# Kernel tuning notes

Hardware: AMD Instinct MI355X
Metric: run time of the kernel (lower is better)

The kernel has to match this reference:

```python
import jax, jax.numpy as jnp
import numpy as np

DIM = 512
HEADS = 8        # MultiHeadAttention default heads=8 (init 'heads' arg actually sets dim_head)
DIM_HEAD = 64    # from AttentionLayers heads=64 passed positionally as dim_head
HIDDEN = HEADS * DIM_HEAD  # 512
EPS = 1e-5


def setup_inputs() -> dict:
    key = jax.random.key(0)
    ks = jax.random.split(key, 8)
    s = 1.0 / np.sqrt(DIM)
    return {
        "x": jax.random.normal(ks[0], (4, 2048, DIM), dtype=jnp.float32),
        "ln_g": jnp.ones((DIM,), dtype=jnp.float32),
        "ln_b": jnp.zeros((DIM,), dtype=jnp.float32),
        "Wq": jax.random.normal(ks[1], (DIM, HIDDEN), dtype=jnp.float32) * s,
        "Wk": jax.random.normal(ks[2], (DIM, HIDDEN), dtype=jnp.float32) * s,
        "Wv": jax.random.normal(ks[3], (DIM, HIDDEN), dtype=jnp.float32) * s,
        "Wo": jax.random.normal(ks[4], (HIDDEN, DIM), dtype=jnp.float32) * s,
        "bo": jnp.zeros((DIM,), dtype=jnp.float32),
    }


def reference(x, ln_g, ln_b, Wq, Wk, Wv, Wo, bo):
    b, n, d = x.shape
    residual = x
    # pre-norm LayerNorm
    mu = jnp.mean(x, axis=-1, keepdims=True)
    var = jnp.mean((x - mu) ** 2, axis=-1, keepdims=True)
    xn = (x - mu) * jax.lax.rsqrt(var + EPS) * ln_g + ln_b
    # QKV projections (no bias), split into heads: [b, s, h, dh]
    q = (xn @ Wq).reshape(b, n, HEADS, DIM_HEAD)
    k = (xn @ Wk).reshape(b, n, HEADS, DIM_HEAD)
    v = (xn @ Wv).reshape(b, n, HEADS, DIM_HEAD)
    scale = HIDDEN ** (-0.5)  # note: scales by hidden_dim, not dim_head (faithful)
    scores = jnp.einsum('bihd,bjhd->bhij', q, k) * scale  # [b,h,i,j] full matrix
    attn = jax.nn.softmax(scores, axis=-1)
    out = jnp.einsum('bhij,bjhd->bihd', attn, v).reshape(b, n, HIDDEN)
    out = out @ Wo + bo
    # residual; the subsequent FFN layer's output is discarded in the source
    return out + residual
```

## Files before the change

kernel.cpp:

```cpp
#include <hip/hip_runtime.h>
#include <hip/hip_bf16.h>

#define DIM 512
#define SEQ 2048
#define BATCH 4
#define NHEADS 8
#define DH 64
#define NROWS (BATCH * SEQ)
#define LN_EPS 1e-5f

typedef __hip_bfloat16 bf16;
typedef __attribute__((ext_vector_type(8))) short short8;
typedef __attribute__((ext_vector_type(4))) float f32x4;

#define MFMA16(a, b, c) __builtin_amdgcn_mfma_f32_16x16x32_bf16((a), (b), (c), 0, 0, 0)

#if __has_builtin(__builtin_amdgcn_exp2f)
#define EXP2(x) __builtin_amdgcn_exp2f(x)
#else
#define EXP2(x) exp2f(x)
#endif

#if defined(__has_builtin)
#if __has_builtin(__builtin_amdgcn_global_load_lds)
#define HAS_GLDS 1
#endif
#endif

__device__ __forceinline__ void glds16(const bf16* g, bf16* l) {
#ifdef HAS_GLDS
  __builtin_amdgcn_global_load_lds((const __attribute__((address_space(1))) void*)g,
                                   (__attribute__((address_space(3))) void*)l, 16, 0, 0);
#else
  *reinterpret_cast<uint4*>(l) = *reinterpret_cast<const uint4*>(g);
#endif
}

__device__ __forceinline__ void store_bf16x4(bf16* p, float a, float b, float c, float d) {
  bf16 tmp[4] = {__float2bfloat16(a), __float2bfloat16(b), __float2bfloat16(c),
                 __float2bfloat16(d)};
  *reinterpret_cast<ushort4*>(p) = *reinterpret_cast<const ushort4*>(tmp);
}

#define B2F(us) __uint_as_float(((unsigned)(us)) << 16)

#define Q_SCALE_LOG2E 0.06375872f

__global__ void setup_kernel(const float* __restrict__ x, const float* __restrict__ gamma,
                             const float* __restrict__ beta, bf16* __restrict__ xn,
                             const float* __restrict__ Wq, const float* __restrict__ Wk,
                             const float* __restrict__ Wv, const float* __restrict__ Wo,
                             bf16* __restrict__ Wt) {
  const int t = threadIdx.x;
  if (blockIdx.x < NROWS / 4) {
    const int row = blockIdx.x * 4 + (t >> 6);
    const int l = t & 63;
    const float4* xr = reinterpret_cast<const float4*>(x + (size_t)row * DIM);
    const float4 v0 = xr[l * 2];
    const float4 v1 = xr[l * 2 + 1];
    float s = (v0.x + v0.y + v0.z + v0.w) + (v1.x + v1.y + v1.z + v1.w);
    float ss = v0.x * v0.x + v0.y * v0.y + v0.z * v0.z + v0.w * v0.w + v1.x * v1.x +
               v1.y * v1.y + v1.z * v1.z + v1.w * v1.w;
#pragma unroll
    for (int off = 1; off < 64; off <<= 1) {
      s += __shfl_xor(s, off);
      ss += __shfl_xor(ss, off);
    }
    const float mu = s * (1.0f / DIM);
    const float rs = rsqrtf(ss * (1.0f / DIM) - mu * mu + LN_EPS);
    const float4 g0 = reinterpret_cast<const float4*>(gamma)[l * 2];
    const float4 g1 = reinterpret_cast<const float4*>(gamma)[l * 2 + 1];
    const float4 b0 = reinterpret_cast<const float4*>(beta)[l * 2];
    const float4 b1 = reinterpret_cast<const float4*>(beta)[l * 2 + 1];
    bf16* o = xn + (size_t)row * DIM + l * 8;
    store_bf16x4(o, (v0.x - mu) * rs * g0.x + b0.x, (v0.y - mu) * rs * g0.y + b0.y,
                 (v0.z - mu) * rs * g0.z + b0.z, (v0.w - mu) * rs * g0.w + b0.w);
    store_bf16x4(o + 4, (v1.x - mu) * rs * g1.x + b1.x, (v1.y - mu) * rs * g1.y + b1.y,
                 (v1.z - mu) * rs * g1.z + b1.z, (v1.w - mu) * rs * g1.w + b1.w);
  } else {
    __shared__ float tile[32][33];
    const int idx = blockIdx.x - NROWS / 4;
    const int bx = idx & 15, by = (idx >> 4) & 15, z = idx >> 8;
    const float* __restrict__ W = (z == 0) ? Wq : (z == 1) ? Wk : (z == 2) ? Wv : Wo;
    const float scale = (z == 0) ? Q_SCALE_LOG2E : 1.0f;
    bf16* __restrict__ dst = Wt + (size_t)z * DIM * DIM;
    const int tx = t & 31, ty = t >> 5;
#pragma unroll
    for (int i = 0; i < 32; i += 8)
      tile[ty + i][tx] = W[(size_t)(by * 32 + ty + i) * DIM + bx * 32 + tx];
    __syncthreads();
#pragma unroll
    for (int i = 0; i < 32; i += 8)
      dst[(size_t)(bx * 32 + ty + i) * DIM + by * 32 + tx] =
          __float2bfloat16(tile[tx][ty + i] * scale);
  }
}

__launch_bounds__(256, 3)
__global__ void gemm_qkv_kernel(const bf16* __restrict__ A, const bf16* __restrict__ Bt,
                                bf16* __restrict__ qo, bf16* __restrict__ ko,
                                bf16* __restrict__ vto) {
  const int m0 = blockIdx.x * 128, n0g = blockIdx.y * 128;
  __shared__ __align__(16) char smem[128 * 136 * 2];
  bf16* const sA = (bf16*)smem;
  bf16* const sB = (bf16*)(smem + 16384);
  bf16* const sT = (bf16*)smem;
  const int t = threadIdx.x, w = t >> 6, l = t & 63;
  const int r = l & 15, g = l >> 4;
  const int wm = w >> 1, wn = w & 1;
  const int crow = w * 32 + (l >> 2);
  const int ccol = (l & 3) * 8;
  const bf16* gA = A + (size_t)(m0 + crow) * DIM + ccol;
  const bf16* gB = Bt + (size_t)(n0g + crow) * DIM + ccol;
  const int loff = w * 1024 + l * 8;
  f32x4 acc[4][4] = {};
  glds16(gA, sA + loff);
  glds16(gA + 16 * DIM, sA + loff + 512);
  glds16(gB, sB + loff);
  glds16(gB + 16 * DIM, sB + loff + 512);
  const int NK = DIM / 32;
  for (int ks = 0; ks < NK; ks++) {
    const int cur = ks & 1;
    __syncthreads();
    if (ks + 1 < NK) {
      const int k0n = (ks + 1) * 32;
      glds16(gA + k0n, sA + (1 - cur) * 4096 + loff);
      glds16(gA + 16 * DIM + k0n, sA + (1 - cur) * 4096 + loff + 512);
      glds16(gB + k0n, sB + (1 - cur) * 4096 + loff);
      glds16(gB + 16 * DIM + k0n, sB + (1 - cur) * 4096 + loff + 512);
    }
    short8 af[4], bfv[4];
#pragma unroll
    for (int i = 0; i < 4; i++)
      af[i] = *reinterpret_cast<const short8*>(
          &sA[cur * 4096 + (wm * 64 + i * 16 + r) * 32 + g * 8]);
#pragma unroll
    for (int j = 0; j < 4; j++)
      bfv[j] = *reinterpret_cast<const short8*>(
          &sB[cur * 4096 + (wn * 64 + j * 16 + r) * 32 + g * 8]);
#pragma unroll
    for (int i = 0; i < 4; i++)
#pragma unroll
      for (int j = 0; j < 4; j++) acc[i][j] = MFMA16(af[i], bfv[j], acc[i][j]);
  }
  const int z = n0g >> 9;
  const int b = m0 / SEQ;
  if (z != 2) {
    bf16* __restrict__ outp = (z == 0) ? qo : ko;
    const int nc0 = (n0g & 511) + wn * 64;
#pragma unroll
    for (int i = 0; i < 4; i++)
#pragma unroll
      for (int j = 0; j < 4; j++)
#pragma unroll
        for (int reg = 0; reg < 4; reg++) {
          const int m = m0 + wm * 64 + i * 16 + g * 4 + reg;
          const int col = nc0 + j * 16 + r;
          outp[(size_t)m * DIM + col] = __float2bfloat16(acc[i][j][reg]);
        }
  } else {
    __syncthreads();
#pragma unroll
    for (int i = 0; i < 4; i++)
#pragma unroll
      for (int j = 0; j < 4; j++)
        store_bf16x4(&sT[(wn * 64 + j * 16 + r) * 136 + wm * 64 + i * 16 + g * 4],
                     acc[i][j][0], acc[i][j][1], acc[i][j][2], acc[i][j][3]);
    __syncthreads();
    const int dr = t >> 1;
    const int mc = (t & 1) * 64;
    const int dcol = (n0g & 511) + dr;
    bf16* dst = vto + ((size_t)b * DIM + dcol) * SEQ + (m0 - b * SEQ) + mc;
#pragma unroll
    for (int uu = 0; uu < 8; uu++)
      *reinterpret_cast<uint4*>(dst + uu * 8) =
          *reinterpret_cast<const uint4*>(&sT[dr * 136 + mc + uu * 8]);
  }
}

template <bool SPLIT>
__launch_bounds__(256, 4)
__global__ void attn_kernel(const bf16* __restrict__ q, const bf16* __restrict__ k,
                            const bf16* __restrict__ vt, bf16* __restrict__ opart,
                            float* __restrict__ lpart) {
  const int bh = blockIdx.x, jh = blockIdx.y, it = blockIdx.z;
  const int b = bh >> 3, h = bh & 7;
  const int t = threadIdx.x, wv = t >> 6, l = t & 63;
  const int r = l & 15, g = l >> 4;
  __shared__ __align__(16) bf16 sK[64 * 64];
  __shared__ __align__(16) bf16 sV[64 * 64];
  __shared__ __align__(16) bf16 sPt[4][2][16][72];
  const int i0 = it * 128 + wv * 32;
  const bf16* qp = q + ((size_t)(b * SEQ) + i0 + r) * DIM + h * DH;
  short8 qf[2][2];
#pragma unroll
  for (int s = 0; s < 2; s++)
#pragma unroll
    for (int kc = 0; kc < 2; kc++)
      qf[s][kc] = *reinterpret_cast<const short8*>(qp + s * 16 * DIM + kc * 32 + g * 8);
  f32x4 oacc[2][4] = {};
  float lsum[2] = {0.f, 0.f};
  const int jbase = SPLIT ? jh * (SEQ / 2) : 0;
  const int srow8 = l >> 3;
  const int u = ((l & 7) - srow8) & 7;
  const bf16* kg = k + ((size_t)(b * SEQ) + jbase + wv * 16 + srow8) * DIM + h * DH + u * 8;
  const bf16* vg = vt + ((size_t)(b * DIM) + h * DH + wv * 16 + srow8) * SEQ + jbase + u * 8;
  const int loff = wv * 1024 + l * 8;
  const int e0 = 64 * r + 8 * ((g + r) & 7);
  const int e1 = 64 * r + 8 * ((4 + g + r) & 7);
  const int NJ = SPLIT ? (SEQ / 2) / 64 : SEQ / 64;
  for (int jt = 0; jt < NJ; jt++) {
    const int j0 = jt * 64;
#pragma unroll
    for (int cc = 0; cc < 2; cc++) {
      glds16(kg + (size_t)(j0 + cc * 8) * DIM, sK + loff + cc * 512);
      glds16(vg + (size_t)(cc * 8) * SEQ + j0, sV + loff + cc * 512);
    }
    __syncthreads();
    f32x4 st[2][4];
#pragma unroll
    for (int c = 0; c < 4; c++) {
      const short8 kf0 = *reinterpret_cast<const short8*>(sK + 1024 * c + e0);
      const short8 kf1 = *reinterpret_cast<const short8*>(sK + 1024 * c + e1);
#pragma unroll
      for (int s = 0; s < 2; s++) {
        f32x4 a = {0.f, 0.f, 0.f, 0.f};
        a = MFMA16(kf0, qf[s][0], a);
        a = MFMA16(kf1, qf[s][1], a);
        st[s][c] = a;
      }
    }
#pragma unroll
    for (int s = 0; s < 2; s++)
#pragma unroll
      for (int c = 0; c < 4; c++) {
        const float p0 = EXP2(st[s][c][0]);
        const float p1 = EXP2(st[s][c][1]);
        const float p2 = EXP2(st[s][c][2]);
        const float p3 = EXP2(st[s][c][3]);
        lsum[s] += (p0 + p1) + (p2 + p3);
        store_bf16x4(&sPt[wv][s][r][c * 16 + g * 4], p0, p1, p2, p3);
      }
#pragma unroll
    for (int kc2 = 0; kc2 < 2; kc2++) {
      short8 pf[2];
#pragma unroll
      for (int s = 0; s < 2; s++)
        pf[s] = *reinterpret_cast<const short8*>(&sPt[wv][s][r][kc2 * 32 + g * 8]);
      const int ev = (kc2 == 0) ? e0 : e1;
#pragma unroll
      for (int dt = 0; dt < 4; dt++) {
        const short8 vf = *reinterpret_cast<const short8*>(sV + 1024 * dt + ev);
#pragma unroll
        for (int s = 0; s < 2; s++) oacc[s][dt] = MFMA16(vf, pf[s], oacc[s][dt]);
      }
    }
    __syncthreads();
  }
#pragma unroll
  for (int s = 0; s < 2; s++) {
    lsum[s] += __shfl_xor(lsum[s], 16);
    lsum[s] += __shfl_xor(lsum[s], 32);
  }
  const size_t obase = ((size_t)(SPLIT ? jh * 32 : 0) + bh) * SEQ;
#pragma unroll
  for (int s = 0; s < 2; s++) {
    const int i = i0 + s * 16 + r;
    if (l < 16) lpart[obase + i] = lsum[s];
#pragma unroll
    for (int dt = 0; dt < 4; dt++)
      store_bf16x4(opart + (obase + i) * 64 + dt * 16 + g * 4, oacc[s][dt][0], oacc[s][dt][1],
                   oacc[s][dt][2], oacc[s][dt][3]);
  }
  if (!SPLIT) {
    const size_t obase1 = ((size_t)32 + bh) * SEQ;
#pragma unroll
    for (int s = 0; s < 2; s++) {
      const int i = i0 + s * 16 + r;
      if (l < 16) lpart[obase1 + i] = 0.f;
#pragma unroll
      for (int dt = 0; dt < 4; dt++)
        store_bf16x4(opart + (obase1 + i) * 64 + dt * 16 + g * 4, 0.f, 0.f, 0.f, 0.f);
    }
  }
}

__launch_bounds__(256, 2)
__global__ void gemm_proj_kernel(const bf16* __restrict__ opart, const float* __restrict__ lpart,
                                 const bf16* __restrict__ Bt, const float* __restrict__ bo,
                                 const float* __restrict__ x, float* __restrict__ out) {
  const int m0 = blockIdx.x * 128, n0 = blockIdx.y * 64;
  __shared__ __align__(16) bf16 sA[128 * 32];
  __shared__ __align__(16) bf16 sB[64 * 32];
  const int t = threadIdx.x, w = t >> 6, l = t & 63;
  const int r = l & 15, g = l >> 4;
  const int wm = w >> 1, wn = w & 1;
  const int arow = t >> 2;
  const int acol = (t & 3) * 8;
  const bf16* gB = Bt + (size_t)(n0 + arow) * DIM + acol;
  f32x4 acc[4][2] = {};
  const int NK = DIM / 32;
  for (int ks = 0; ks < NK; ks++) {
    const int k0 = ks * 32;
    const int h = k0 >> 6;
    const int d0 = (k0 & 63) + acol;
    uint4 areg[2];
#pragma unroll
    for (int c = 0; c < 2; c++) {
      const int m = m0 + c * 64 + arow;
      const int bb = m >> 11, ii = m & 2047;
      const size_t row0 = ((size_t)(bb * 8 + h)) * SEQ + ii;
      const size_t row1 = row0 + (size_t)32 * SEQ;
      const uint4 A0 = *reinterpret_cast<const uint4*>(opart + row0 * 64 + d0);
      const uint4 A1 = *reinterpret_cast<const uint4*>(opart + row1 * 64 + d0);
      const float inv = 1.0f / (lpart[row0] + lpart[row1]);
      const ushort* a0 = (const ushort*)&A0;
      const ushort* a1 = (const ushort*)&A1;
      bf16 rr[8];
#pragma unroll
      for (int e = 0; e < 8; e++)
        rr[e] = __float2bfloat16((B2F(a0[e]) + B2F(a1[e])) * inv);
      areg[c] = *reinterpret_cast<const uint4*>(rr);
    }
    const uint4 breg = *reinterpret_cast<const uint4*>(gB + k0);
    __syncthreads();
    *reinterpret_cast<uint4*>(&sA[(0 * 64 + arow) * 32 + acol]) = areg[0];
    *reinterpret_cast<uint4*>(&sA[(1 * 64 + arow) * 32 + acol]) = areg[1];
    *reinterpret_cast<uint4*>(&sB[arow * 32 + acol]) = breg;
    __syncthreads();
    short8 af[4], bfv[2];
#pragma unroll
    for (int i = 0; i < 4; i++)
      af[i] = *reinterpret_cast<const short8*>(&sA[(wm * 64 + i * 16 + r) * 32 + g * 8]);
#pragma unroll
    for (int j = 0; j < 2; j++)
      bfv[j] = *reinterpret_cast<const short8*>(&sB[(wn * 32 + j * 16 + r) * 32 + g * 8]);
#pragma unroll
    for (int i = 0; i < 4; i++)
#pragma unroll
      for (int j = 0; j < 2; j++) acc[i][j] = MFMA16(af[i], bfv[j], acc[i][j]);
  }
#pragma unroll
  for (int i = 0; i < 4; i++)
#pragma unroll
    for (int j = 0; j < 2; j++)
#pragma unroll
      for (int reg = 0; reg < 4; reg++) {
        const int m = m0 + wm * 64 + i * 16 + g * 4 + reg;
        const int col = n0 + wn * 32 + j * 16 + r;
        out[(size_t)m * DIM + col] = acc[i][j][reg] + bo[col] + x[(size_t)m * DIM + col];
      }
}

extern "C" void kernel_launch(void* const* d_in, const int* in_sizes, int n_in,
                              void* d_out, int out_size, void* d_ws, size_t ws_size,
                              hipStream_t stream) {
  (void)in_sizes; (void)n_in; (void)out_size;
  const float* x    = (const float*)d_in[0];
  const float* ln_g = (const float*)d_in[1];
  const float* ln_b = (const float*)d_in[2];
  const float* Wq   = (const float*)d_in[3];
  const float* Wk   = (const float*)d_in[4];
  const float* Wv   = (const float*)d_in[5];
  const float* Wo   = (const float*)d_in[6];
  const float* bo   = (const float*)d_in[7];
  float* out = (float*)d_out;
  char* ws = (char*)d_ws;
  bf16* xn  = (bf16*)(ws);
  bf16* wt  = (bf16*)(ws + (8u << 20));
  bf16* qb  = (bf16*)(ws + (10u << 20));
  bf16* kb  = (bf16*)(ws + (18u << 20));
  bf16* vtb = (bf16*)(ws + (26u << 20));
  bf16* opart = (bf16*)(ws + (34u << 20));
  float* lpart = (float*)(ws + (50u << 20));
  const bool split = ws_size >= ((50u << 20) + (1u << 19));

  setup_kernel<<<NROWS / 4 + 1024, 256, 0, stream>>>(x, ln_g, ln_b, xn, Wq, Wk, Wv, Wo, wt);
  gemm_qkv_kernel<<<dim3(NROWS / 128, (3 * DIM) / 128), 256, 0, stream>>>(xn, wt, qb, kb, vtb);
  if (split) {
    attn_kernel<true><<<dim3(BATCH * NHEADS, 2, SEQ / 128), 256, 0, stream>>>(
        qb, kb, vtb, opart, lpart);
  } else {
    attn_kernel<false><<<dim3(BATCH * NHEADS, 1, SEQ / 128), 256, 0, stream>>>(
        qb, kb, vtb, opart, lpart);
  }
  gemm_proj_kernel<<<dim3(NROWS / 128, DIM / 64), 256, 0, stream>>>(
      opart, lpart, wt + 3 * DIM * DIM, bo, x, out);
}
```

Before: 167.3 us.

## Rewrite attention inner loop with 32x32 MFMA, register P, double-buffered K/V

The attention kernel switches from 16x16x32 to 32x32x16 bf16 MFMA, with each wave handling 64 query rows, so a block covers 256 rows and the grid's z dimension is halved. The probability tile is repacked in registers with cross-half shuffles instead of a round trip through shared memory. K/V tiles are double-buffered so the next tile's global-to-LDS load overlaps compute, using a single raw barrier per iteration. The aim is higher MFMA throughput and fewer LDS accesses and syncs, at the cost of more registers (launch bounds drop to 2 blocks per CU) and fewer blocks in the grid.

```diff
diff --git a/kernel.cpp b/kernel.cpp
--- a/kernel.cpp
+++ b/kernel.cpp
@@ -12,8 +12,10 @@
 typedef __hip_bfloat16 bf16;
 typedef __attribute__((ext_vector_type(8))) short short8;
 typedef __attribute__((ext_vector_type(4))) float f32x4;
+typedef __attribute__((ext_vector_type(16))) float f32x16;
 
 #define MFMA16(a, b, c) __builtin_amdgcn_mfma_f32_16x16x32_bf16((a), (b), (c), 0, 0, 0)
+#define MFMA32(a, b, c) __builtin_amdgcn_mfma_f32_32x32x16_bf16((a), (b), (c), 0, 0, 0)
 
 #if __has_builtin(__builtin_amdgcn_exp2f)
 #define EXP2(x) __builtin_amdgcn_exp2f(x)
@@ -42,7 +44,23 @@
   *reinterpret_cast<ushort4*>(p) = *reinterpret_cast<const ushort4*>(tmp);
 }
 
+__device__ __forceinline__ unsigned pk2(float a, float b) {
+  union { bf16 h[2]; unsigned u; } x;
+  x.h[0] = __float2bfloat16(a);
+  x.h[1] = __float2bfloat16(b);
+  return x.u;
+}
+
+__device__ __forceinline__ short8 mk8(unsigned a, unsigned b, unsigned c, unsigned d) {
+  union { unsigned u[4]; short8 s; } x;
+  x.u[0] = a; x.u[1] = b; x.u[2] = c; x.u[3] = d;
+  return x.s;
+}
+
 #define B2F(us) __uint_as_float(((unsigned)(us)) << 16)
+
+#define BARRIER() asm volatile("s_barrier" ::: "memory")
+#define WAITVM0() asm volatile("s_waitcnt vmcnt(0)" ::: "memory")
 
 #define Q_SCALE_LOG2E 0.06375872f
 
@@ -179,108 +197,141 @@
 }
 
 template <bool SPLIT>
-__launch_bounds__(256, 4)
+__launch_bounds__(256, 2)
 __global__ void attn_kernel(const bf16* __restrict__ q, const bf16* __restrict__ k,
                             const bf16* __restrict__ vt, bf16* __restrict__ opart,
                             float* __restrict__ lpart) {
   const int bh = blockIdx.x, jh = blockIdx.y, it = blockIdx.z;
   const int b = bh >> 3, h = bh & 7;
   const int t = threadIdx.x, wv = t >> 6, l = t & 63;
-  const int r = l & 15, g = l >> 4;
-  __shared__ __align__(16) bf16 sK[64 * 64];
-  __shared__ __align__(16) bf16 sV[64 * 64];
-  __shared__ __align__(16) bf16 sPt[4][2][16][72];
-  const int i0 = it * 128 + wv * 32;
-  const bf16* qp = q + ((size_t)(b * SEQ) + i0 + r) * DIM + h * DH;
-  short8 qf[2][2];
-#pragma unroll
-  for (int s = 0; s < 2; s++)
-#pragma unroll
-    for (int kc = 0; kc < 2; kc++)
-      qf[s][kc] = *reinterpret_cast<const short8*>(qp + s * 16 * DIM + kc * 32 + g * 8);
-  f32x4 oacc[2][4] = {};
-  float lsum[2] = {0.f, 0.f};
+  const int c2 = l & 31, h2 = l >> 5;
+  __shared__ __align__(16) bf16 sK[2][64 * 64];
+  __shared__ __align__(16) bf16 sV[2][64 * 64];
+  const int i0w = it * 256 + wv * 64;
   const int jbase = SPLIT ? jh * (SEQ / 2) : 0;
+
   const int srow8 = l >> 3;
   const int u = ((l & 7) - srow8) & 7;
   const bf16* kg = k + ((size_t)(b * SEQ) + jbase + wv * 16 + srow8) * DIM + h * DH + u * 8;
   const bf16* vg = vt + ((size_t)(b * DIM) + h * DH + wv * 16 + srow8) * SEQ + jbase + u * 8;
   const int loff = wv * 1024 + l * 8;
-  const int e0 = 64 * r + 8 * ((g + r) & 7);
-  const int e1 = 64 * r + 8 * ((4 + g + r) & 7);
+#pragma unroll
+  for (int cc = 0; cc < 2; cc++) {
+    glds16(kg + (size_t)(cc * 8) * DIM, &sK[0][loff + cc * 512]);
+    glds16(vg + (size_t)(cc * 8) * SEQ, &sV[0][loff + cc * 512]);
+  }
+
+  const bf16* qp = q + ((size_t)(b * SEQ) + i0w + c2) * DIM + h * DH + h2 * 8;
+  short8 qf[2][4];
+#pragma unroll
+  for (int x = 0; x < 2; x++)
+#pragma unroll
+    for (int kk = 0; kk < 4; kk++)
+      qf[x][kk] = *reinterpret_cast<const short8*>(qp + x * 32 * DIM + kk * 16);
+
+  int eo[4];
+#pragma unroll
+  for (int x = 0; x < 4; x++) eo[x] = c2 * 64 + 8 * ((2 * x + h2 + c2) & 7);
+
+  f32x16 oacc[2][2] = {};
+  float lsum[2] = {0.f, 0.f};
   const int NJ = SPLIT ? (SEQ / 2) / 64 : SEQ / 64;
+
   for (int jt = 0; jt < NJ; jt++) {
-    const int j0 = jt * 64;
-#pragma unroll
-    for (int cc = 0; cc < 2; cc++) {
-      glds16(kg + (size_t)(j0 + cc * 8) * DIM, sK + loff + cc * 512);
-      glds16(vg + (size_t)(cc * 8) * SEQ + j0, sV + loff + cc * 512);
-    }
-    __syncthreads();
-    f32x4 st[2][4];
-#pragma unroll
-    for (int c = 0; c < 4; c++) {
-      const short8 kf0 = *reinterpret_cast<const short8*>(sK + 1024 * c + e0);
-      const short8 kf1 = *reinterpret_cast<const short8*>(sK + 1024 * c + e1);
-#pragma unroll
-      for (int s = 0; s < 2; s++) {
-        f32x4 a = {0.f, 0.f, 0.f, 0.f};
-        a = MFMA16(kf0, qf[s][0], a);
-        a = MFMA16(kf1, qf[s][1], a);
-        st[s][c] = a;
+    WAITVM0();
+    BARRIER();
+    if (jt + 1 < NJ) {
+      const int j0n = (jt + 1) * 64;
+      const int bn = (jt + 1) & 1;
+#pragma unroll
+      for (int cc = 0; cc < 2; cc++) {
+        glds16(kg + (size_t)(j0n + cc * 8) * DIM, &sK[bn][loff + cc * 512]);
+        glds16(vg + (size_t)(cc * 8) * SEQ + j0n, &sV[bn][loff + cc * 512]);
       }
     }
-#pragma unroll
-    for (int s = 0; s < 2; s++)
-#pragma unroll
-      for (int c = 0; c < 4; c++) {
-        const float p0 = EXP2(st[s][c][0]);
-        const float p1 = EXP2(st[s][c][1]);
-        const float p2 = EXP2(st[s][c][2]);
-        const float p3 = EXP2(st[s][c][3]);
-        lsum[s] += (p0 + p1) + (p2 + p3);
-        store_bf16x4(&sPt[wv][s][r][c * 16 + g * 4], p0, p1, p2, p3);
+    const bf16* sKb = sK[jt & 1];
+    const bf16* sVb = sV[jt & 1];
+#pragma unroll
+    for (int jb = 0; jb < 2; jb++) {
+      short8 kf[4];
+#pragma unroll
+      for (int kk = 0; kk < 4; kk++)
+        kf[kk] = *reinterpret_cast<const short8*>(sKb + jb * 2048 + eo[kk]);
+      f32x16 st[2] = {};
+#pragma unroll
+      for (int kk = 0; kk < 4; kk++) {
+        st[0] = MFMA32(kf[kk], qf[0][kk], st[0]);
+        st[1] = MFMA32(kf[kk], qf[1][kk], st[1]);
       }
-#pragma unroll
-    for (int kc2 = 0; kc2 < 2; kc2++) {
-      short8 pf[2];
-#pragma unroll
-      for (int s = 0; s < 2; s++)
-        pf[s] = *reinterpret_cast<const short8*>(&sPt[wv][s][r][kc2 * 32 + g * 8]);
-      const int ev = (kc2 == 0) ? e0 : e1;
-#pragma unroll
-      for (int dt = 0; dt < 4; dt++) {
-        const short8 vf = *reinterpret_cast<const short8*>(sV + 1024 * dt + ev);
-#pragma unroll
-        for (int s = 0; s < 2; s++) oacc[s][dt] = MFMA16(vf, pf[s], oacc[s][dt]);
+      short8 pf[2][2];
+#pragma unroll
+      for (int x = 0; x < 2; x++) {
+        float p[16];
+#pragma unroll
+        for (int e = 0; e < 16; e++) p[e] = EXP2(st[x][e]);
+        lsum[x] += ((((p[0] + p[1]) + (p[2] + p[3])) + ((p[4] + p[5]) + (p[6] + p[7]))) +
+                    (((p[8] + p[9]) + (p[10] + p[11])) + ((p[12] + p[13]) + (p[14] + p[15]))));
+        unsigned W[4][2];
+#pragma unroll
+        for (int a = 0; a < 4; a++)
+#pragma unroll
+          for (int w = 0; w < 2; w++) W[a][w] = pk2(p[4 * a + 2 * w], p[4 * a + 2 * w + 1]);
+#pragma unroll
+        for (int k2 = 0; k2 < 2; k2++) {
+          unsigned F0, F1, F2, F3;
+          {
+            const unsigned We = W[2 * k2][0], Wo = W[2 * k2 + 1][0];
+            const unsigned te = __shfl_xor(We, 32), to = __shfl_xor(Wo, 32);
+            F0 = h2 ? to : We;
+            F2 = h2 ? Wo : te;
+          }
+          {
+            const unsigned We = W[2 * k2][1], Wo = W[2 * k2 + 1][1];
+            const unsigned te = __shfl_xor(We, 32), to = __shfl_xor(Wo, 32);
+            F1 = h2 ? to : We;
+            F3 = h2 ? Wo : te;
+          }
+          pf[x][k2] = mk8(F0, F1, F2, F3);
+        }
       }
-    }
-    __syncthreads();
-  }
-#pragma unroll
-  for (int s = 0; s < 2; s++) {
-    lsum[s] += __shfl_xor(lsum[s], 16);
-    lsum[s] += __shfl_xor(lsum[s], 32);
+#pragma unroll
+      for (int j2 = 0; j2 < 2; j2++) {
+#pragma unroll
+        for (int db = 0; db < 2; db++) {
+          const short8 vf =
+              *reinterpret_cast<const short8*>(sVb + db * 2048 + eo[2 * jb + j2]);
+          oacc[0][db] = MFMA32(vf, pf[0][j2], oacc[0][db]);
+          oacc[1][db] = MFMA32(vf, pf[1][j2], oacc[1][db]);
+        }
+      }
+    }
   }
   const size_t obase = ((size_t)(SPLIT ? jh * 32 : 0) + bh) * SEQ;
 #pragma unroll
-  for (int s = 0; s < 2; s++) {
-    const int i = i0 + s * 16 + r;
-    if (l < 16) lpart[obase + i] = lsum[s];
-#pragma unroll
-    for (int dt = 0; dt < 4; dt++)
-      store_bf16x4(opart + (obase + i) * 64 + dt * 16 + g * 4, oacc[s][dt][0], oacc[s][dt][1],
-                   oacc[s][dt][2], oacc[s][dt][3]);
+  for (int x = 0; x < 2; x++) {
+    lsum[x] += __shfl_xor(lsum[x], 32);
+    const int i = i0w + x * 32 + c2;
+    if (l < 32) lpart[obase + i] = lsum[x];
+#pragma unroll
+    for (int db = 0; db < 2; db++)
+#pragma unroll
+      for (int rr = 0; rr < 4; rr++)
+        store_bf16x4(opart + (obase + i) * 64 + db * 32 + rr * 8 + h2 * 4,
+                     oacc[x][db][4 * rr + 0], oacc[x][db][4 * rr + 1],
+                     oacc[x][db][4 * rr + 2], oacc[x][db][4 * rr + 3]);
   }
   if (!SPLIT) {
     const size_t obase1 = ((size_t)32 + bh) * SEQ;
 #pragma unroll
-    for (int s = 0; s < 2; s++) {
-      const int i = i0 + s * 16 + r;
-      if (l < 16) lpart[obase1 + i] = 0.f;
-#pragma unroll
-      for (int dt = 0; dt < 4; dt++)
-        store_bf16x4(opart + (obase1 + i) * 64 + dt * 16 + g * 4, 0.f, 0.f, 0.f, 0.f);
+    for (int x = 0; x < 2; x++) {
+      const int i = i0w + x * 32 + c2;
+      if (l < 32) lpart[obase1 + i] = 0.f;
+#pragma unroll
+      for (int db = 0; db < 2; db++)
+#pragma unroll
+        for (int rr = 0; rr < 4; rr++)
+          store_bf16x4(opart + (obase1 + i) * 64 + db * 32 + rr * 8 + h2 * 4, 0.f, 0.f, 0.f,
+                       0.f);
     }
   }
 }
@@ -378,10 +429,10 @@
   setup_kernel<<<NROWS / 4 + 1024, 256, 0, stream>>>(x, ln_g, ln_b, xn, Wq, Wk, Wv, Wo, wt);
   gemm_qkv_kernel<<<dim3(NROWS / 128, (3 * DIM) / 128), 256, 0, stream>>>(xn, wt, qb, kb, vtb);
   if (split) {
-    attn_kernel<true><<<dim3(BATCH * NHEADS, 2, SEQ / 128), 256, 0, stream>>>(
+    attn_kernel<true><<<dim3(BATCH * NHEADS, 2, SEQ / 256), 256, 0, stream>>>(
         qb, kb, vtb, opart, lpart);
   } else {
-    attn_kernel<false><<<dim3(BATCH * NHEADS, 1, SEQ / 128), 256, 0, stream>>>(
+    attn_kernel<false><<<dim3(BATCH * NHEADS, 1, SEQ / 256), 256, 0, stream>>>(
         qb, kb, vtb, opart, lpart);
   }
   gemm_proj_kernel<<<dim3(NROWS / 128, DIM / 64), 256, 0, stream>>>(
```

New measurement: 170.0 us. No clear change (+1.6%).

## Double-buffer K/V tiles in attention loop to overlap loads with MFMA

Applied to the files above, without the earlier changes.

Splits the K and V shared-memory tiles into two buffers and issues the global-to-LDS loads for the next tile right after the barrier, so they overlap with the current tile's score and PV computation. Raw s_waitcnt/s_barrier asm replaces __syncthreads, and launch bounds drop from 4 to 3 blocks per CU to cover the larger LDS footprint. The prologue is odd: it loads the first K chunk twice to the same slot and patches the second chunk inside the loop at jt==0. Fewer resident blocks and hand-written barriers could cut latency hiding or risk races.

```diff
diff --git a/kernel.cpp b/kernel.cpp
--- a/kernel.cpp
+++ b/kernel.cpp
@@ -43,6 +43,9 @@
 }
 
 #define B2F(us) __uint_as_float(((unsigned)(us)) << 16)
+
+#define BARRIER() asm volatile("s_barrier" ::: "memory")
+#define WAITVM0() asm volatile("s_waitcnt vmcnt(0)" ::: "memory")
 
 #define Q_SCALE_LOG2E 0.06375872f
 
@@ -179,7 +182,7 @@
 }
 
 template <bool SPLIT>
-__launch_bounds__(256, 4)
+__launch_bounds__(256, 3)
 __global__ void attn_kernel(const bf16* __restrict__ q, const bf16* __restrict__ k,
                             const bf16* __restrict__ vt, bf16* __restrict__ opart,
                             float* __restrict__ lpart) {
@@ -187,8 +190,8 @@
   const int b = bh >> 3, h = bh & 7;
   const int t = threadIdx.x, wv = t >> 6, l = t & 63;
   const int r = l & 15, g = l >> 4;
-  __shared__ __align__(16) bf16 sK[64 * 64];
-  __shared__ __align__(16) bf16 sV[64 * 64];
+  __shared__ __align__(16) bf16 sK[2][64 * 64];
+  __shared__ __align__(16) bf16 sV[2][64 * 64];
   __shared__ __align__(16) bf16 sPt[4][2][16][72];
   const int i0 = it * 128 + wv * 32;
   const bf16* qp = q + ((size_t)(b * SEQ) + i0 + r) * DIM + h * DH;
@@ -209,19 +212,33 @@
   const int e0 = 64 * r + 8 * ((g + r) & 7);
   const int e1 = 64 * r + 8 * ((4 + g + r) & 7);
   const int NJ = SPLIT ? (SEQ / 2) / 64 : SEQ / 64;
+#pragma unroll
+  for (int cc = 0; cc < 2; cc++) {
+    glds16(kg, &sK[0][loff + cc * 512]);
+    glds16(vg + (size_t)(cc * 8) * SEQ, &sV[0][loff + cc * 512]);
+  }
   for (int jt = 0; jt < NJ; jt++) {
-    const int j0 = jt * 64;
-#pragma unroll
-    for (int cc = 0; cc < 2; cc++) {
-      glds16(kg + (size_t)(j0 + cc * 8) * DIM, sK + loff + cc * 512);
-      glds16(vg + (size_t)(cc * 8) * SEQ + j0, sV + loff + cc * 512);
-    }
-    __syncthreads();
+    if (jt == 0) {
+      glds16(kg + (size_t)8 * DIM, &sK[0][loff + 512]);
+    }
+    WAITVM0();
+    BARRIER();
+    if (jt + 1 < NJ) {
+      const int j0n = (jt + 1) * 64;
+      const int bn = (jt + 1) & 1;
+#pragma unroll
+      for (int cc = 0; cc < 2; cc++) {
+        glds16(kg + (size_t)(j0n + cc * 8) * DIM, &sK[bn][loff + cc * 512]);
+        glds16(vg + (size_t)(cc * 8) * SEQ + j0n, &sV[bn][loff + cc * 512]);
+      }
+    }
+    const bf16* sKb = sK[jt & 1];
+    const bf16* sVb = sV[jt & 1];
     f32x4 st[2][4];
 #pragma unroll
     for (int c = 0; c < 4; c++) {
-      const short8 kf0 = *reinterpret_cast<const short8*>(sK + 1024 * c + e0);
-      const short8 kf1 = *reinterpret_cast<const short8*>(sK + 1024 * c + e1);
+      const short8 kf0 = *reinterpret_cast<const short8*>(sKb + 1024 * c + e0);
+      const short8 kf1 = *reinterpret_cast<const short8*>(sKb + 1024 * c + e1);
 #pragma unroll
       for (int s = 0; s < 2; s++) {
         f32x4 a = {0.f, 0.f, 0.f, 0.f};
@@ -250,12 +267,12 @@
       const int ev = (kc2 == 0) ? e0 : e1;
 #pragma unroll
       for (int dt = 0; dt < 4; dt++) {
-        const short8 vf = *reinterpret_cast<const short8*>(sV + 1024 * dt + ev);
+        const short8 vf = *reinterpret_cast<const short8*>(sVb + 1024 * dt + ev);
 #pragma unroll
         for (int s = 0; s < 2; s++) oacc[s][dt] = MFMA16(vf, pf[s], oacc[s][dt]);
       }
     }
-    __syncthreads();
+    BARRIER();
   }
 #pragma unroll
   for (int s = 0; s < 2; s++) {
```

Measured after the change: 174.4 us. 1.04x slower.

## Double-buffer K/V tiles in attention and retile output projection GEMM

Applied to the files above, without the earlier changes.

The attention loop now walks the keys in 32-wide tiles held in two LDS buffers. The next tile is prefetched with global_load_lds while the current one is computed, and a single raw s_barrier plus vmcnt wait per iteration replaces the two __syncthreads. The output projection GEMM changes from 128x64 to 64x128 tiles and loads B directly into LDS. Its launch bound rises to 4 blocks per CU. The raw barrier relies on each wave waiting for its own LDS writes, and with smaller tiles there are more loop iterations to pay overhead on.

```diff
diff --git a/kernel.cpp b/kernel.cpp
--- a/kernel.cpp
+++ b/kernel.cpp
@@ -43,6 +43,9 @@
 }
 
 #define B2F(us) __uint_as_float(((unsigned)(us)) << 16)
+
+#define BARRIER() asm volatile("s_barrier" ::: "memory")
+#define WAITVM0() asm volatile("s_waitcnt vmcnt(0)" ::: "memory")
 
 #define Q_SCALE_LOG2E 0.06375872f
 
@@ -187,8 +190,8 @@
   const int b = bh >> 3, h = bh & 7;
   const int t = threadIdx.x, wv = t >> 6, l = t & 63;
   const int r = l & 15, g = l >> 4;
-  __shared__ __align__(16) bf16 sK[64 * 64];
-  __shared__ __align__(16) bf16 sV[64 * 64];
+  __shared__ __align__(16) bf16 sK[2][32 * 64];
+  __shared__ __align__(16) bf16 sV[2][64 * 32];
   __shared__ __align__(16) bf16 sPt[4][2][16][72];
   const int i0 = it * 128 + wv * 32;
   const bf16* qp = q + ((size_t)(b * SEQ) + i0 + r) * DIM + h * DH;
@@ -201,27 +204,35 @@
   f32x4 oacc[2][4] = {};
   float lsum[2] = {0.f, 0.f};
   const int jbase = SPLIT ? jh * (SEQ / 2) : 0;
-  const int srow8 = l >> 3;
-  const int u = ((l & 7) - srow8) & 7;
-  const bf16* kg = k + ((size_t)(b * SEQ) + jbase + wv * 16 + srow8) * DIM + h * DH + u * 8;
-  const bf16* vg = vt + ((size_t)(b * DIM) + h * DH + wv * 16 + srow8) * SEQ + jbase + u * 8;
-  const int loff = wv * 1024 + l * 8;
-  const int e0 = 64 * r + 8 * ((g + r) & 7);
-  const int e1 = 64 * r + 8 * ((4 + g + r) & 7);
-  const int NJ = SPLIT ? (SEQ / 2) / 64 : SEQ / 64;
+  const int kr8 = l >> 3;
+  const int ku = ((l & 7) - kr8) & 7;
+  const bf16* kg = k + ((size_t)(b * SEQ) + jbase + wv * 8 + kr8) * DIM + h * DH + ku * 8;
+  const int vr4 = l >> 2;
+  const int vu = ((l & 3) - ((l >> 3) & 3)) & 3;
+  const bf16* vg = vt + ((size_t)(b * DIM) + h * DH + wv * 16 + vr4) * SEQ + jbase + vu * 8;
+  const int loff = wv * 512 + l * 8;
+  glds16(kg, &sK[0][loff]);
+  glds16(vg, &sV[0][loff]);
+  const int ek0 = r * 64 + 8 * ((g + r) & 7);
+  const int ek1 = r * 64 + 8 * ((g + 4 + r) & 7);
+  const int ev = r * 32 + 8 * ((g + (r >> 1)) & 3);
+  const int NJ = (SPLIT ? SEQ / 2 : SEQ) / 32;
   for (int jt = 0; jt < NJ; jt++) {
-    const int j0 = jt * 64;
-#pragma unroll
-    for (int cc = 0; cc < 2; cc++) {
-      glds16(kg + (size_t)(j0 + cc * 8) * DIM, sK + loff + cc * 512);
-      glds16(vg + (size_t)(cc * 8) * SEQ + j0, sV + loff + cc * 512);
-    }
-    __syncthreads();
-    f32x4 st[2][4];
-#pragma unroll
-    for (int c = 0; c < 4; c++) {
-      const short8 kf0 = *reinterpret_cast<const short8*>(sK + 1024 * c + e0);
-      const short8 kf1 = *reinterpret_cast<const short8*>(sK + 1024 * c + e1);
+    WAITVM0();
+    BARRIER();
+    if (jt + 1 < NJ) {
+      const int j0n = (jt + 1) * 32;
+      const int bn = (jt + 1) & 1;
+      glds16(kg + (size_t)j0n * DIM, &sK[bn][loff]);
+      glds16(vg + j0n, &sV[bn][loff]);
+    }
+    const bf16* sKb = sK[jt & 1];
+    const bf16* sVb = sV[jt & 1];
+    f32x4 st[2][2];
+#pragma unroll
+    for (int c = 0; c < 2; c++) {
+      const short8 kf0 = *reinterpret_cast<const short8*>(sKb + 1024 * c + ek0);
+      const short8 kf1 = *reinterpret_cast<const short8*>(sKb + 1024 * c + ek1);
 #pragma unroll
       for (int s = 0; s < 2; s++) {
         f32x4 a = {0.f, 0.f, 0.f, 0.f};
@@ -233,7 +244,7 @@
 #pragma unroll
     for (int s = 0; s < 2; s++)
 #pragma unroll
-      for (int c = 0; c < 4; c++) {
+      for (int c = 0; c < 2; c++) {
         const float p0 = EXP2(st[s][c][0]);
         const float p1 = EXP2(st[s][c][1]);
         const float p2 = EXP2(st[s][c][2]);
@@ -241,21 +252,16 @@
         lsum[s] += (p0 + p1) + (p2 + p3);
         store_bf16x4(&sPt[wv][s][r][c * 16 + g * 4], p0, p1, p2, p3);
       }
-#pragma unroll
-    for (int kc2 = 0; kc2 < 2; kc2++) {
-      short8 pf[2];
-#pragma unroll
-      for (int s = 0; s < 2; s++)
-        pf[s] = *reinterpret_cast<const short8*>(&sPt[wv][s][r][kc2 * 32 + g * 8]);
-      const int ev = (kc2 == 0) ? e0 : e1;
-#pragma unroll
-      for (int dt = 0; dt < 4; dt++) {
-        const short8 vf = *reinterpret_cast<const short8*>(sV + 1024 * dt + ev);
-#pragma unroll
-        for (int s = 0; s < 2; s++) oacc[s][dt] = MFMA16(vf, pf[s], oacc[s][dt]);
-      }
-    }
-    __syncthreads();
+    short8 pf[2];
+#pragma unroll
+    for (int s = 0; s < 2; s++)
+      pf[s] = *reinterpret_cast<const short8*>(&sPt[wv][s][r][g * 8]);
+#pragma unroll
+    for (int dt = 0; dt < 4; dt++) {
+      const short8 vf = *reinterpret_cast<const short8*>(sVb + 512 * dt + ev);
+#pragma unroll
+      for (int s = 0; s < 2; s++) oacc[s][dt] = MFMA16(vf, pf[s], oacc[s][dt]);
+    }
   }
 #pragma unroll
   for (int s = 0; s < 2; s++) {
@@ -285,69 +291,64 @@
   }
 }
 
-__launch_bounds__(256, 2)
+__launch_bounds__(256, 4)
 __global__ void gemm_proj_kernel(const bf16* __restrict__ opart, const float* __restrict__ lpart,
                                  const bf16* __restrict__ Bt, const float* __restrict__ bo,
                                  const float* __restrict__ x, float* __restrict__ out) {
-  const int m0 = blockIdx.x * 128, n0 = blockIdx.y * 64;
-  __shared__ __align__(16) bf16 sA[128 * 32];
-  __shared__ __align__(16) bf16 sB[64 * 32];
+  const int m0 = blockIdx.x * 64, n0 = blockIdx.y * 128;
+  __shared__ __align__(16) bf16 sA[64 * 32];
+  __shared__ __align__(16) bf16 sB[128 * 32];
   const int t = threadIdx.x, w = t >> 6, l = t & 63;
   const int r = l & 15, g = l >> 4;
   const int wm = w >> 1, wn = w & 1;
   const int arow = t >> 2;
   const int acol = (t & 3) * 8;
-  const bf16* gB = Bt + (size_t)(n0 + arow) * DIM + acol;
-  f32x4 acc[4][2] = {};
+  const bf16* gB = Bt + (size_t)(n0 + w * 32 + (l >> 2)) * DIM + (l & 3) * 8;
+  f32x4 acc[2][4] = {};
   const int NK = DIM / 32;
   for (int ks = 0; ks < NK; ks++) {
     const int k0 = ks * 32;
     const int h = k0 >> 6;
     const int d0 = (k0 & 63) + acol;
-    uint4 areg[2];
-#pragma unroll
-    for (int c = 0; c < 2; c++) {
-      const int m = m0 + c * 64 + arow;
-      const int bb = m >> 11, ii = m & 2047;
-      const size_t row0 = ((size_t)(bb * 8 + h)) * SEQ + ii;
-      const size_t row1 = row0 + (size_t)32 * SEQ;
-      const uint4 A0 = *reinterpret_cast<const uint4*>(opart + row0 * 64 + d0);
-      const uint4 A1 = *reinterpret_cast<const uint4*>(opart + row1 * 64 + d0);
-      const float inv = 1.0f / (lpart[row0] + lpart[row1]);
-      const ushort* a0 = (const ushort*)&A0;
-      const ushort* a1 = (const ushort*)&A1;
-      bf16 rr[8];
-#pragma unroll
-      for (int e = 0; e < 8; e++)
-        rr[e] = __float2bfloat16((B2F(a0[e]) + B2F(a1[e])) * inv);
-      areg[c] = *reinterpret_cast<const uint4*>(rr);
-    }
-    const uint4 breg = *reinterpret_cast<const uint4*>(gB + k0);
-    __syncthreads();
-    *reinterpret_cast<uint4*>(&sA[(0 * 64 + arow) * 32 + acol]) = areg[0];
-    *reinterpret_cast<uint4*>(&sA[(1 * 64 + arow) * 32 + acol]) = areg[1];
-    *reinterpret_cast<uint4*>(&sB[arow * 32 + acol]) = breg;
-    __syncthreads();
-    short8 af[4], bfv[2];
-#pragma unroll
-    for (int i = 0; i < 4; i++)
-      af[i] = *reinterpret_cast<const short8*>(&sA[(wm * 64 + i * 16 + r) * 32 + g * 8]);
-#pragma unroll
-    for (int j = 0; j < 2; j++)
-      bfv[j] = *reinterpret_cast<const short8*>(&sB[(wn * 32 + j * 16 + r) * 32 + g * 8]);
-#pragma unroll
-    for (int i = 0; i < 4; i++)
-#pragma unroll
-      for (int j = 0; j < 2; j++) acc[i][j] = MFMA16(af[i], bfv[j], acc[i][j]);
-  }
-#pragma unroll
-  for (int i = 0; i < 4; i++)
-#pragma unroll
-    for (int j = 0; j < 2; j++)
+    const int m = m0 + arow;
+    const int bb = m >> 11, ii = m & 2047;
+    const size_t row0 = ((size_t)(bb * 8 + h)) * SEQ + ii;
+    const size_t row1 = row0 + (size_t)32 * SEQ;
+    const uint4 A0 = *reinterpret_cast<const uint4*>(opart + row0 * 64 + d0);
+    const uint4 A1 = *reinterpret_cast<const uint4*>(opart + row1 * 64 + d0);
+    const float inv = 1.0f / (lpart[row0] + lpart[row1]);
+    const ushort* a0 = (const ushort*)&A0;
+    const ushort* a1 = (const ushort*)&A1;
+    bf16 rr[8];
+#pragma unroll
+    for (int e = 0; e < 8; e++)
+      rr[e] = __float2bfloat16((B2F(a0[e]) + B2F(a1[e])) * inv);
+    const uint4 areg = *reinterpret_cast<const uint4*>(rr);
+    __syncthreads();
+    *reinterpret_cast<uint4*>(&sA[arow * 32 + acol]) = areg;
+    glds16(gB + k0, sB + w * 1024 + l * 8);
+    glds16(gB + 16 * DIM + k0, sB + w * 1024 + 512 + l * 8);
+    __syncthreads();
+    short8 af[2], bfv[4];
+#pragma unroll
+    for (int i = 0; i < 2; i++)
+      af[i] = *reinterpret_cast<const short8*>(&sA[(wm * 32 + i * 16 + r) * 32 + g * 8]);
+#pragma unroll
+    for (int j = 0; j < 4; j++)
+      bfv[j] = *reinterpret_cast<const short8*>(&sB[(wn * 64 + j * 16 + r) * 32 + g * 8]);
+#pragma unroll
+    for (int i = 0; i < 2; i++)
+#pragma unroll
+      for (int j = 0; j < 4; j++) acc[i][j] = MFMA16(af[i], bfv[j], acc[i][j]);
+  }
+#pragma unroll
+  for (int i = 0; i < 2; i++)
+#pragma unroll
+    for (int j = 0; j < 4; j++)
 #pragma unroll
       for (int reg = 0; reg < 4; reg++) {
-        const int m = m0 + wm * 64 + i * 16 + g * 4 + reg;
-        const int col = n0 + wn * 32 + j * 16 + r;
+        const int m = m0 + wm * 32 + i * 16 + g * 4 + reg;
+        const int col = n0 + wn * 64 + j * 16 + r;
         out[(size_t)m * DIM + col] = acc[i][j][reg] + bo[col] + x[(size_t)m * DIM + col];
       }
 }
@@ -384,6 +385,6 @@
     attn_kernel<false><<<dim3(BATCH * NHEADS, 1, SEQ / 128), 256, 0, stream>>>(
         qb, kb, vtb, opart, lpart);
   }
-  gemm_proj_kernel<<<dim3(NROWS / 128, DIM / 64), 256, 0, stream>>>(
+  gemm_proj_kernel<<<dim3(NROWS / 64, DIM / 128), 256, 0, stream>>>(
       opart, lpart, wt + 3 * DIM * DIM, bo, x, out);
 }
```

Result: faster. 161.9 us (-3.3%).
